# Optimization experiments

Hardware: AMD Instinct MI355X
Metric: run time of the kernel (lower is better)

## Reference

```python
import jax, jax.numpy as jnp
import numpy as np

EPS = 1e-6
SINKHORN_ITERS = 8
TEMPERATURE = 1.0
B, N, D = 4, 8192, 512
E, OUT = 8, 512
H = 1


def setup_inputs() -> dict:
    key = jax.random.key(0)
    k1, k2, k3 = jax.random.split(key, 3)
    x = jax.random.normal(k1, (B, N, D), dtype=jnp.float32)
    gate_weight = jax.random.normal(k2, (H, D, E), dtype=jnp.float32)
    experts = jax.random.normal(k3, (E, D, OUT), dtype=jnp.float32) * 0.02
    return {"x": x, "gate_weight": gate_weight, "experts": experts}


def _sinkhorn(logits):
    # logits: (b, h, n, e). log(clamp(.,eps)) then alternating row/col log-normalization.
    t = jnp.log(jnp.clip(logits, EPS)) / TEMPERATURE
    for _ in range(SINKHORN_ITERS):
        t = t - jax.nn.logsumexp(t, axis=-2, keepdims=True)  # normalize over tokens n
        t = t - jax.nn.logsumexp(t, axis=-1, keepdims=True)  # normalize over experts e
    return jnp.exp(t)


def reference(x, gate_weight, experts):
    b, n, d = x.shape
    e = experts.shape[0]
    m = n // e  # tokens per expert
    xh = x[:, None, :, :]  # b 1 n d  (single-headed -> h=1)
    gate_logits = jnp.einsum('bhnd,hde->bhne', xh, gate_weight)
    gates = _sinkhorn(gate_logits)  # b h n e
    # topk over token dim n, per expert: move n to last axis for lax.top_k
    g_t = jnp.swapaxes(gates, -1, -2)  # b h e n
    vals, idx = jax.lax.top_k(g_t, m)  # (b h e m), (b h e m)
    gate_values = jnp.transpose(vals, (2, 0, 1, 3))[..., None]  # e b h m 1
    # gather routed tokens: routed[e,b,h,m,d] = x[b,h,idx[b,h,e,m],d]
    routed = jnp.take_along_axis(xh[:, :, None, :, :], idx[..., None], axis=3)  # b h e m d
    routed = jnp.transpose(routed, (2, 0, 1, 3, 4))  # e b h m d
    expert_w = experts[:, None, :, :]  # e h i o with h=1 (rearrange 'e i o -> e 1 i o')
    outputs = jnp.einsum('ebhmi,ehio->ebhmo', routed, expert_w)  # e b h m o
    outputs = outputs * gate_values
    # scatter back (set semantics, matching einx set_at)
    bh_idx = idx.reshape(b, 1, e * m)  # b h (e m)
    bh_vals = jnp.transpose(outputs, (1, 2, 0, 3, 4)).reshape(b, 1, e * m, outputs.shape[-1])
    def scat(i1, v1):
        return jnp.zeros((n, v1.shape[-1]), dtype=v1.dtype).at[i1].set(v1)
    routed_back = jax.vmap(jax.vmap(scat))(bh_idx, bh_vals)  # b h n o
    return routed_back[:, 0]  # b n o
```

## Files before the change

kernel.cpp:

```cpp
#include <hip/hip_runtime.h>
#include <hip/hip_bf16.h>

#define BB 4
#define NN 8192
#define DD 512
#define EE 8
#define OUTD 512
#define TOPM 1024
#define EPSV 1e-6f
#define ITERS 8

using s16x8 = __attribute__((ext_vector_type(8))) short;
using f32x4 = __attribute__((ext_vector_type(4))) float;
typedef unsigned long long u64;

__device__ __forceinline__ unsigned short f2bf(float f) {
  unsigned u = __float_as_uint(f);
  return (unsigned short)((u + 0x7FFFu + ((u >> 16) & 1u)) >> 16);
}

__device__ __forceinline__ void gll16(const void* g, void* l) {
  __builtin_amdgcn_global_load_lds((const __attribute__((address_space(1))) void*)g,
                                   (__attribute__((address_space(3))) void*)l, 16, 0, 0);
}

__global__ __launch_bounds__(256) void k_gate(const float* __restrict__ x,
                                              const float* __restrict__ gw,
                                              float* __restrict__ t0,
                                              unsigned short* __restrict__ xbf,
                                              int* __restrict__ eo,
                                              int* __restrict__ counts,
                                              const float* __restrict__ W,
                                              unsigned short* __restrict__ WT) {
  const int tid = threadIdx.x;
  if (blockIdx.x >= 2048) {
    __shared__ float tl[32][33];
    const int widx = blockIdx.x - 2048;
    const int e = widx >> 8, rem = widx & 255;
    const int k0 = (rem >> 4) * 32, n0 = (rem & 15) * 32;
    const int ty = tid >> 5, tx = tid & 31;
    const float* src = W + ((long)e * DD + k0) * OUTD + n0;
#pragma unroll
    for (int j = 0; j < 4; ++j)
      tl[ty + j * 8][tx] = src[(long)(ty + j * 8) * OUTD + tx];
    __syncthreads();
    unsigned short* dst = WT + ((long)e * OUTD + n0) * DD + k0;
#pragma unroll
    for (int j = 0; j < 4; ++j)
      dst[(long)(ty + j * 8) * DD + tx] = f2bf(tl[tx][ty + j * 8]);
    return;
  }
  if (tid < 16) eo[blockIdx.x * 16 + tid] = -1;
  if (blockIdx.x == 0 && tid >= 64 && tid < 64 + BB * EE) counts[tid - 64] = 0;
  const int lane = tid & 63;
  const int w    = tid >> 6;
  float4 g0[8], g1[8];
  const float* gb = gw + (lane * 8) * EE;
#pragma unroll
  for (int q = 0; q < 8; ++q) {
    g0[q] = *(const float4*)(gb + q * EE);
    g1[q] = *(const float4*)(gb + q * EE + 4);
  }
  const long row0 = (long)blockIdx.x * 16 + w * 4;
  float4 xa[4], xb[4];
#pragma unroll
  for (int i = 0; i < 4; ++i) {
    const float* xr = x + (row0 + i) * DD + lane * 8;
    xa[i] = *(const float4*)(xr);
    xb[i] = *(const float4*)(xr + 4);
  }
  float vout[4];
#pragma unroll
  for (int i = 0; i < 4; ++i) {
    float xv[8] = {xa[i].x, xa[i].y, xa[i].z, xa[i].w,
                   xb[i].x, xb[i].y, xb[i].z, xb[i].w};
    s16x8 xo;
#pragma unroll
    for (int j = 0; j < 8; ++j) xo[j] = (short)f2bf(xv[j]);
    *(s16x8*)(xbf + (row0 + i) * DD + lane * 8) = xo;

    float acc[8] = {0.f,0.f,0.f,0.f,0.f,0.f,0.f,0.f};
#pragma unroll
    for (int q = 0; q < 8; ++q) {
      acc[0] += xv[q] * g0[q].x; acc[1] += xv[q] * g0[q].y;
      acc[2] += xv[q] * g0[q].z; acc[3] += xv[q] * g0[q].w;
      acc[4] += xv[q] * g1[q].x; acc[5] += xv[q] * g1[q].y;
      acc[6] += xv[q] * g1[q].z; acc[7] += xv[q] * g1[q].w;
    }
    const bool o1 = lane & 1;
    float own, oth, b0, b1, b2, b3, c0, c1, v;
    own = o1 ? acc[1] : acc[0]; oth = o1 ? acc[0] : acc[1];
    b0 = own + __shfl_xor(oth, 1);
    own = o1 ? acc[3] : acc[2]; oth = o1 ? acc[2] : acc[3];
    b1 = own + __shfl_xor(oth, 1);
    own = o1 ? acc[5] : acc[4]; oth = o1 ? acc[4] : acc[5];
    b2 = own + __shfl_xor(oth, 1);
    own = o1 ? acc[7] : acc[6]; oth = o1 ? acc[6] : acc[7];
    b3 = own + __shfl_xor(oth, 1);
    const bool o2 = lane & 2;
    own = o2 ? b1 : b0; oth = o2 ? b0 : b1;
    c0 = own + __shfl_xor(oth, 2);
    own = o2 ? b3 : b2; oth = o2 ? b2 : b3;
    c1 = own + __shfl_xor(oth, 2);
    const bool o4 = lane & 4;
    own = o4 ? c1 : c0; oth = o4 ? c0 : c1;
    v = own + __shfl_xor(oth, 4);
    v += __shfl_xor(v, 8);
    v += __shfl_xor(v, 16);
    v += __shfl_xor(v, 32);
    vout[i] = v;
  }
  const int gsel = lane >> 3;
  float vsel = vout[0];
  vsel = (gsel == 1) ? vout[1] : vsel;
  vsel = (gsel == 2) ? vout[2] : vsel;
  vsel = (gsel == 3) ? vout[3] : vsel;
  if (lane < 32) t0[row0 * EE + lane] = logf(fmaxf(vsel, EPSV));
}

__global__ __launch_bounds__(1024) void k_sink5(const float* __restrict__ t0,
                                                float* __restrict__ R,
                                                float* __restrict__ C) {
  const int b = blockIdx.x;
  const int tid = threadIdx.x;
  const int wv = tid >> 6, ln = tid & 63;
  const float* tb = t0 + (long)b * NN * EE;
  float E[8][8], u[8], dl[8];
  __shared__ float ws[16][8];
  __shared__ float Csh[8];
  __shared__ float Ssh[8];
#pragma unroll
  for (int j = 0; j < 8; ++j) {
    const float* p = tb + (long)(j * 1024 + tid) * EE;
    float4 a = *(const float4*)p, b4 = *(const float4*)(p + 4);
    E[j][0] = expf(a.x);  E[j][1] = expf(a.y);
    E[j][2] = expf(a.z);  E[j][3] = expf(a.w);
    E[j][4] = expf(b4.x); E[j][5] = expf(b4.y);
    E[j][6] = expf(b4.z); E[j][7] = expf(b4.w);
    u[j] = 1.f;
  }
  for (int it = 0; it < ITERS; ++it) {
    float P[8] = {0.f,0.f,0.f,0.f,0.f,0.f,0.f,0.f};
#pragma unroll
    for (int j = 0; j < 8; ++j)
#pragma unroll
      for (int e = 0; e < 8; ++e) P[e] += E[j][e] * u[j];
#pragma unroll
    for (int d = 1; d <= 4; d <<= 1) {
#pragma unroll
      for (int e = 0; e < 8; ++e) {
        float tmp = __shfl_xor(P[e], d);
        P[e] += ((ln & d) == (e & d)) ? tmp : 0.f;
      }
    }
    float pv = P[0];
#pragma unroll
    for (int e = 1; e < 8; ++e) pv = ((ln & 7) == e) ? P[e] : pv;
#pragma unroll
    for (int d = 8; d < 64; d <<= 1) pv += __shfl_xor(pv, d);
    if (ln < 8) ws[wv][ln] = pv;
    __syncthreads();
    if (tid < 64) {
      const int q = ln >> 3, e = ln & 7;
      float s = ws[q][e] + ws[q + 8][e];
#pragma unroll
      for (int d = 8; d < 64; d <<= 1) s += __shfl_xor(s, d);
      if (ln < 8) { Csh[ln] = 1.f / s; Ssh[ln] = s; }
    }
    __syncthreads();
    float vv[8];
#pragma unroll
    for (int e = 0; e < 8; ++e) vv[e] = Csh[e];
#pragma unroll
    for (int j = 0; j < 8; ++j) {
      float d0 = E[j][0] * vv[0];
#pragma unroll
      for (int e = 1; e < 8; ++e) d0 += E[j][e] * vv[e];
      dl[j] = d0;
      u[j] = 1.f / d0;
    }
    __syncthreads();
  }
#pragma unroll
  for (int j = 0; j < 8; ++j) R[(long)b * NN + j * 1024 + tid] = logf(dl[j]);
  if (tid < 8) C[b * EE + tid] = logf(Ssh[tid]);
}

__global__ __launch_bounds__(1024) void k_topk(const float* __restrict__ t0,
                                               const float* __restrict__ R,
                                               int* __restrict__ expert_of) {
  __shared__ unsigned key[NN];
  __shared__ int hist[256];
  __shared__ int bcast[2];
  __shared__ int wsum[16];
  const int b = blockIdx.x >> 3, e = blockIdx.x & 7;
  const int tid = threadIdx.x;
  const int wv = tid >> 6, ln = tid & 63;
  const float* t = t0 + (long)b * NN * EE + e;
  const float* Rb = R + b * NN;
  for (int n = tid; n < NN; n += 1024) {
    float f = t[n * EE] - Rb[n];
    unsigned u = __float_as_uint(f);
    u = (u & 0x80000000u) ? ~u : (u | 0x80000000u);
    key[n] = u;
  }
  __syncthreads();
  unsigned prefix = 0, mask = 0;
  int k = TOPM;
  for (int shift = 24; shift >= 0; shift -= 8) {
    if (tid < 256) hist[tid] = 0;
    __syncthreads();
    for (int n = tid; n < NN; n += 1024) {
      unsigned u = key[n];
      if ((u & mask) == prefix) atomicAdd(&hist[(u >> shift) & 255], 1);
    }
    __syncthreads();
    for (int d = 1; d < 256; d <<= 1) {
      int add = 0;
      if (tid < 256 - d) add = hist[tid + d];
      __syncthreads();
      if (tid < 256) hist[tid] += add;
      __syncthreads();
    }
    if (tid < 256) {
      int sv = hist[tid];
      int sv1 = (tid < 255) ? hist[tid + 1] : 0;
      if (sv >= k && sv1 < k) { bcast[0] = k - sv1; bcast[1] = tid; }
    }
    __syncthreads();
    k = bcast[0];
    prefix |= ((unsigned)bcast[1]) << shift;
    mask |= (255u << shift);
    __syncthreads();
  }
  const unsigned theta = prefix;
  const int need = k;
  const int base = tid * 8;
  int c = 0;
#pragma unroll
  for (int j = 0; j < 8; ++j) if (key[base + j] == theta) ++c;
  int inc = c;
#pragma unroll
  for (int d = 1; d < 64; d <<= 1) {
    int o = __shfl_up(inc, d);
    if (ln >= d) inc += o;
  }
  if (ln == 63) wsum[wv] = inc;
  __syncthreads();
  if (tid == 0) {
    int runv = 0;
    for (int i = 0; i < 16; ++i) { int t2 = wsum[i]; wsum[i] = runv; runv += t2; }
  }
  __syncthreads();
  int run = wsum[wv] + inc - c;
  int* eo = expert_of + b * NN;
  for (int j = 0; j < 8; ++j) {
    int n = base + j;
    unsigned u = key[n];
    bool sel = false;
    if (u > theta) sel = true;
    else if (u == theta) { if (run < need) sel = true; ++run; }
    if (sel) atomicMax(&eo[n], e);
  }
}

__global__ __launch_bounds__(256) void k_build(const int* __restrict__ expert_of,
                                               const float* __restrict__ t0,
                                               const float* __restrict__ R,
                                               const float* __restrict__ C,
                                               int* __restrict__ counts,
                                               int* __restrict__ lists,
                                               float* __restrict__ gvals) {
  __shared__ int hist8[8], base8[8];
  const int tid = threadIdx.x;
  if (tid < 8) hist8[tid] = 0;
  __syncthreads();
  const long i = (long)blockIdx.x * 256 + tid;
  const int b = (int)(i >> 13);
  const int e = expert_of[i];
  int lpos = -1;
  if (e >= 0) lpos = atomicAdd(&hist8[e], 1);
  __syncthreads();
  if (tid < 8 && hist8[tid] > 0)
    base8[tid] = atomicAdd(&counts[b * EE + tid], hist8[tid]);
  __syncthreads();
  if (e >= 0) {
    const int n = (int)(i & (NN - 1));
    const int be = b * EE + e;
    const int slot = be * TOPM + base8[e] + lpos;
    lists[slot] = n;
    gvals[slot] = expf(t0[i * EE + e] - C[be] - R[i]);
  }
}

__global__ __launch_bounds__(256) void k_zero(const int* __restrict__ eo,
                                              float* __restrict__ out) {
  const int row = blockIdx.x * 4 + (threadIdx.x >> 6);
  if (eo[row] >= 0) return;
  const int ln = threadIdx.x & 63;
  float4 z = make_float4(0.f, 0.f, 0.f, 0.f);
  float4* p = (float4*)(out + (long)row * OUTD) + ln;
  p[0] = z; p[64] = z;
}

__global__ __launch_bounds__(256) void k_gemm(const unsigned short* __restrict__ xbf,
                                              const unsigned short* __restrict__ WT,
                                              const int* __restrict__ counts,
                                              const int* __restrict__ lists,
                                              const float* __restrict__ gvals,
                                              float* __restrict__ out) {
  const int id = blockIdx.x;
  const int xq = id >> 8;
  const int be = (id >> 3) & 31;
  const int yq = id & 7;
  const int b = be >> 3, e = be & 7;
  const int cnt = counts[be];
  const int r0 = yq * 128;
  if (r0 >= cnt) return;
  const int c0 = xq * 128;

  __shared__ unsigned short As[128 * 64];
  __shared__ unsigned short Bs[128 * 64];
  __shared__ int   rowTok[128];
  __shared__ float rowG[128];

  const int tid = threadIdx.x;
  if (tid < 128) {
    int r = r0 + tid;
    rowTok[tid] = (r < cnt) ? lists[be * TOPM + r] : -1;
    rowG[tid]   = (r < cnt) ? gvals[be * TOPM + r] : 0.f;
  }
  __syncthreads();

  const int w = tid >> 6, l = tid & 63;
  const int rbase = w * 32 + (l >> 3);
  const int sL = l & 7;
  const unsigned short* xb_b = xbf + (long)b * NN * DD;
  const unsigned short* wt_e = WT + (long)e * OUTD * DD;
  int tokc[4]; int sGa[4], sGb[4];
#pragma unroll
  for (int c = 0; c < 4; ++c) {
    int r = rbase + c * 8;
    int tk = rowTok[r]; if (tk < 0) tk = 0;
    tokc[c] = tk;
    sGa[c] = (sL ^ (r & 7)) * 8;
    sGb[c] = sGa[c];
  }

  const int wr = w >> 1, wc = w & 1;
  const int fr = l & 15, fq = l >> 4;
  int aoff[4][2], boff[4][2];
#pragma unroll
  for (int m = 0; m < 4; ++m) {
#pragma unroll
    for (int kk = 0; kk < 2; ++kk) {
      int row = wr * 64 + m * 16 + fr;
      aoff[m][kk] = row * 64 + (((fq + 4 * kk) ^ (row & 7)) * 8);
      int col = wc * 64 + m * 16 + fr;
      boff[m][kk] = col * 64 + (((fq + 4 * kk) ^ (col & 7)) * 8);
    }
  }

  f32x4 acc[4][4] = {};

#define STAGE(kb) {                                                          \
    int ko = (kb) * 64;                                                      \
    _Pragma("unroll")                                                        \
    for (int c = 0; c < 4; ++c) {                                            \
      int r = rbase + c * 8;                                                 \
      gll16(xb_b + (long)tokc[c] * DD + ko + sGa[c],                         \
            As + (w * 32 + c * 8) * 64);                                     \
      gll16(wt_e + (long)(c0 + r) * DD + ko + sGb[c],                        \
            Bs + (w * 32 + c * 8) * 64);                                     \
    }                                                                        \
  }

  STAGE(0);
  for (int kb = 0; kb < 8; ++kb) {
    __syncthreads();
    s16x8 af[4][2], bf_[4][2];
#pragma unroll
    for (int m = 0; m < 4; ++m) {
      af[m][0] = *(const s16x8*)(As + aoff[m][0]);
      af[m][1] = *(const s16x8*)(As + aoff[m][1]);
      bf_[m][0] = *(const s16x8*)(Bs + boff[m][0]);
      bf_[m][1] = *(const s16x8*)(Bs + boff[m][1]);
    }
    __syncthreads();
    if (kb < 7) STAGE(kb + 1);
#pragma unroll
    for (int kk = 0; kk < 2; ++kk)
#pragma unroll
      for (int m = 0; m < 4; ++m)
#pragma unroll
        for (int n = 0; n < 4; ++n)
          acc[m][n] = __builtin_amdgcn_mfma_f32_16x16x32_bf16(af[m][kk], bf_[n][kk], acc[m][n], 0, 0, 0);
  }
#undef STAGE

#pragma unroll
  for (int m = 0; m < 4; ++m) {
    int rbase2 = wr * 64 + m * 16 + fq * 4;
    int tok[4]; float g[4];
#pragma unroll
    for (int j = 0; j < 4; ++j) { tok[j] = rowTok[rbase2 + j]; g[j] = rowG[rbase2 + j]; }
#pragma unroll
    for (int n = 0; n < 4; ++n) {
      int col = c0 + wc * 64 + n * 16 + fr;
#pragma unroll
      for (int j = 0; j < 4; ++j) {
        if (tok[j] >= 0)
          out[((long)b * NN + tok[j]) * OUTD + col] = acc[m][n][j] * g[j];
      }
    }
  }
}

extern "C" void kernel_launch(void* const* d_in, const int* in_sizes, int n_in,
                              void* d_out, int out_size, void* d_ws, size_t ws_size,
                              hipStream_t stream) {
  const float* x  = (const float*)d_in[0];
  const float* gw = (const float*)d_in[1];
  const float* ex = (const float*)d_in[2];
  float* out = (float*)d_out;

  char* wsb = (char*)d_ws;
  float*          t0     = (float*)(wsb);
  unsigned short* xbf    = (unsigned short*)(wsb + (1l << 20));
  unsigned short* WT     = (unsigned short*)(wsb + (33l << 20));
  const long base = 37l << 20;
  float*          R      = (float*)(wsb + base);
  int*            eo     = (int*)  (wsb + base + (128l << 10));
  int*            lists  = (int*)  (wsb + base + (256l << 10));
  float*          gvals  = (float*)(wsb + base + (384l << 10));
  float*          C      = (float*)(wsb + base + (512l << 10));
  int*            counts = (int*)  (wsb + base + (512l << 10) + 1024);

  k_gate<<<2048 + 2048, 256, 0, stream>>>(x, gw, t0, xbf, eo, counts, ex, WT);
  k_sink5<<<BB, 1024, 0, stream>>>(t0, R, C);
  k_topk<<<BB * EE, 1024, 0, stream>>>(t0, R, eo);
  k_build<<<(BB * NN) / 256, 256, 0, stream>>>(eo, t0, R, C, counts, lists, gvals);
  k_zero<<<(BB * NN) / 4, 256, 0, stream>>>(eo, out);
  k_gemm<<<1024, 256, 0, stream>>>(xbf, WT, counts, lists, gvals, out);
}
```

Measured before the change: 114.3 us.

## Widen GEMM tile to full output width with double-buffered LDS K-loop

The expert GEMM now has each 512-thread block compute a 128-row by 512-column tile, so each gathered token row is loaded from x once instead of four times. The K loop uses 32-wide slices with double-buffered LDS, issuing the next global-to-LDS load before the current slice's MFMAs and dropping one barrier per iteration. The grid shrinks from 1024 to 256 blocks, which lowers parallelism and raises accumulator register pressure (32 f32x4 per lane).

Result: slower. 117.0 us (+2.3%).

```diff
diff --git a/kernel.cpp b/kernel.cpp
--- a/kernel.cpp
+++ b/kernel.cpp
@@ -303,24 +303,23 @@
   p[0] = z; p[64] = z;
 }
 
-__global__ __launch_bounds__(256) void k_gemm(const unsigned short* __restrict__ xbf,
-                                              const unsigned short* __restrict__ WT,
-                                              const int* __restrict__ counts,
-                                              const int* __restrict__ lists,
-                                              const float* __restrict__ gvals,
-                                              float* __restrict__ out) {
+__global__ __launch_bounds__(512, 2) void k_gemm(const unsigned short* __restrict__ xbf,
+                                                 const unsigned short* __restrict__ WT,
+                                                 const int* __restrict__ counts,
+                                                 const int* __restrict__ lists,
+                                                 const float* __restrict__ gvals,
+                                                 float* __restrict__ out) {
   const int id = blockIdx.x;
-  const int xq = id >> 8;
-  const int be = (id >> 3) & 31;
-  const int yq = id & 7;
-  const int b = be >> 3, e = be & 7;
+  const int e = id & 7;
+  const int b = (id >> 3) & 3;
+  const int yq = id >> 5;
+  const int be = b * EE + e;
   const int cnt = counts[be];
   const int r0 = yq * 128;
   if (r0 >= cnt) return;
-  const int c0 = xq * 128;
-
-  __shared__ unsigned short As[128 * 64];
-  __shared__ unsigned short Bs[128 * 64];
+
+  __shared__ unsigned short As[2][128 * 32];
+  __shared__ unsigned short Bs[2][512 * 32];
   __shared__ int   rowTok[128];
   __shared__ float rowG[128];
 
@@ -333,80 +332,67 @@
   __syncthreads();
 
   const int w = tid >> 6, l = tid & 63;
-  const int rbase = w * 32 + (l >> 3);
-  const int sL = l & 7;
-  const unsigned short* xb_b = xbf + (long)b * NN * DD;
+  const int raS = w * 16 + (l >> 2);
+  int tokA = rowTok[raS]; if (tokA < 0) tokA = 0;
+  const unsigned short* gA = xbf + ((long)b * NN + tokA) * DD + (((l & 3) ^ (raS & 3)) * 8);
   const unsigned short* wt_e = WT + (long)e * OUTD * DD;
-  int tokc[4]; int sGa[4], sGb[4];
+  const unsigned short* gB[4];
 #pragma unroll
   for (int c = 0; c < 4; ++c) {
-    int r = rbase + c * 8;
-    int tk = rowTok[r]; if (tk < 0) tk = 0;
-    tokc[c] = tk;
-    sGa[c] = (sL ^ (r & 7)) * 8;
-    sGb[c] = sGa[c];
-  }
-
-  const int wr = w >> 1, wc = w & 1;
+    int rb = c * 128 + w * 16 + (l >> 2);
+    gB[c] = wt_e + (long)rb * DD + (((l & 3) ^ (rb & 3)) * 8);
+  }
+
   const int fr = l & 15, fq = l >> 4;
-  int aoff[4][2], boff[4][2];
-#pragma unroll
-  for (int m = 0; m < 4; ++m) {
-#pragma unroll
-    for (int kk = 0; kk < 2; ++kk) {
-      int row = wr * 64 + m * 16 + fr;
-      aoff[m][kk] = row * 64 + (((fq + 4 * kk) ^ (row & 7)) * 8);
-      int col = wc * 64 + m * 16 + fr;
-      boff[m][kk] = col * 64 + (((fq + 4 * kk) ^ (col & 7)) * 8);
-    }
-  }
-
-  f32x4 acc[4][4] = {};
-
-#define STAGE(kb) {                                                          \
-    int ko = (kb) * 64;                                                      \
-    _Pragma("unroll")                                                        \
-    for (int c = 0; c < 4; ++c) {                                            \
-      int r = rbase + c * 8;                                                 \
-      gll16(xb_b + (long)tokc[c] * DD + ko + sGa[c],                         \
-            As + (w * 32 + c * 8) * 64);                                     \
-      gll16(wt_e + (long)(c0 + r) * DD + ko + sGb[c],                        \
-            Bs + (w * 32 + c * 8) * 64);                                     \
-    }                                                                        \
-  }
-
-  STAGE(0);
-  for (int kb = 0; kb < 8; ++kb) {
-    __syncthreads();
-    s16x8 af[4][2], bf_[4][2];
-#pragma unroll
-    for (int m = 0; m < 4; ++m) {
-      af[m][0] = *(const s16x8*)(As + aoff[m][0]);
-      af[m][1] = *(const s16x8*)(As + aoff[m][1]);
-      bf_[m][0] = *(const s16x8*)(Bs + boff[m][0]);
-      bf_[m][1] = *(const s16x8*)(Bs + boff[m][1]);
-    }
-    __syncthreads();
-    if (kb < 7) STAGE(kb + 1);
-#pragma unroll
-    for (int kk = 0; kk < 2; ++kk)
-#pragma unroll
-      for (int m = 0; m < 4; ++m)
-#pragma unroll
-        for (int n = 0; n < 4; ++n)
-          acc[m][n] = __builtin_amdgcn_mfma_f32_16x16x32_bf16(af[m][kk], bf_[n][kk], acc[m][n], 0, 0, 0);
+  int aoff[8], boff[4];
+#pragma unroll
+  for (int m = 0; m < 8; ++m) {
+    int row = m * 16 + fr;
+    aoff[m] = row * 32 + ((fq ^ (row & 3)) * 8);
+  }
+#pragma unroll
+  for (int n = 0; n < 4; ++n) {
+    int col = w * 64 + n * 16 + fr;
+    boff[n] = col * 32 + ((fq ^ (col & 3)) * 8);
+  }
+
+  f32x4 acc[8][4] = {};
+
+#define STAGE(kb, p) {                                                        \
+    int ko = (kb) * 32;                                                       \
+    gll16(gA + ko, &As[p][(w * 16) * 32]);                                    \
+    _Pragma("unroll")                                                         \
+    for (int c = 0; c < 4; ++c)                                               \
+      gll16(gB[c] + ko, &Bs[p][(c * 128 + w * 16) * 32]);                     \
+  }
+
+  STAGE(0, 0);
+  for (int kb = 0; kb < 16; ++kb) {
+    const int p = kb & 1;
+    __syncthreads();
+    if (kb < 15) STAGE(kb + 1, p ^ 1);
+    s16x8 af[8], bf_[4];
+#pragma unroll
+    for (int m = 0; m < 8; ++m) af[m] = *(const s16x8*)(&As[p][0] + aoff[m]);
+#pragma unroll
+    for (int n = 0; n < 4; ++n) bf_[n] = *(const s16x8*)(&Bs[p][0] + boff[n]);
+#pragma unroll
+    for (int m = 0; m < 8; ++m)
+#pragma unroll
+      for (int n = 0; n < 4; ++n)
+        acc[m][n] = __builtin_amdgcn_mfma_f32_16x16x32_bf16(af[m], bf_[n], acc[m][n], 0, 0, 0);
   }
 #undef STAGE
 
 #pragma unroll
-  for (int m = 0; m < 4; ++m) {
-    int rbase2 = wr * 64 + m * 16 + fq * 4;
+  for (int m = 0; m < 8; ++m) {
+    int rb2 = m * 16 + fq * 4;
     int tok[4]; float g[4];
 #pragma unroll
-    for (int j = 0; j < 4; ++j) { tok[j] = rowTok[rbase2 + j]; g[j] = rowG[rbase2 + j]; }
+    for (int j = 0; j < 4; ++j) { tok[j] = rowTok[rb2 + j]; g[j] = rowG[rb2 + j]; }
 #pragma unroll
     for (int n = 0; n < 4; ++n) {
-      int col = c0 + wc * 64 + n * 16 + fr;
+      int col = w * 64 + n * 16 + fr;
 #pragma unroll
       for (int j = 0; j < 4; ++j) {
         if (tok[j] >= 0)
@@ -441,5 +427,5 @@
   k_topk<<<BB * EE, 1024, 0, stream>>>(t0, R, eo);
   k_build<<<(BB * NN) / 256, 256, 0, stream>>>(eo, t0, R, C, counts, lists, gvals);
   k_zero<<<(BB * NN) / 4, 256, 0, stream>>>(eo, out);
-  k_gemm<<<1024, 256, 0, stream>>>(xbf, WT, counts, lists, gvals, out);
-}
+  k_gemm<<<256, 512, 0, stream>>>(xbf, WT, counts, lists, gvals, out);
+}
```

## Fuse build and zero kernels, speed up top-k radix select scan, flatten gate weights

Applied to the files above, without the earlier changes.

Merges the list-building and output-zeroing kernels into one launch so the two no longer run back to back. The radix-select histogram scan in k_topk now uses a single-wave shuffle suffix scan instead of a barrier-heavy 256-thread Hillis-Steele scan, and the first-pass histogram is built while the keys are written. Gate weights are loaded into a flat register array pinned with asm barriers. The intent is fewer launches and fewer block-wide syncs, at the cost of higher register pressure in k_gate and a heterogeneous fused kernel.

After: 107.0 us. -6.4%, faster.

```diff
diff --git a/kernel.cpp b/kernel.cpp
--- a/kernel.cpp
+++ b/kernel.cpp
@@ -54,13 +54,17 @@
   if (blockIdx.x == 0 && tid >= 64 && tid < 64 + BB * EE) counts[tid - 64] = 0;
   const int lane = tid & 63;
   const int w    = tid >> 6;
-  float4 g0[8], g1[8];
+  float gwf[64];
   const float* gb = gw + (lane * 8) * EE;
 #pragma unroll
-  for (int q = 0; q < 8; ++q) {
-    g0[q] = *(const float4*)(gb + q * EE);
-    g1[q] = *(const float4*)(gb + q * EE + 4);
-  }
+  for (int q = 0; q < 16; ++q) {
+    float4 t = *(const float4*)(gb + q * 4);
+    gwf[q * 4 + 0] = t.x; gwf[q * 4 + 1] = t.y;
+    gwf[q * 4 + 2] = t.z; gwf[q * 4 + 3] = t.w;
+  }
+#pragma unroll
+  for (int q = 0; q < 64; ++q) asm volatile("" : "+v"(gwf[q]));
+
   const long row0 = (long)blockIdx.x * 16 + w * 4;
   float4 xa[4], xb[4];
 #pragma unroll
@@ -81,12 +85,9 @@
 
     float acc[8] = {0.f,0.f,0.f,0.f,0.f,0.f,0.f,0.f};
 #pragma unroll
-    for (int q = 0; q < 8; ++q) {
-      acc[0] += xv[q] * g0[q].x; acc[1] += xv[q] * g0[q].y;
-      acc[2] += xv[q] * g0[q].z; acc[3] += xv[q] * g0[q].w;
-      acc[4] += xv[q] * g1[q].x; acc[5] += xv[q] * g1[q].y;
-      acc[6] += xv[q] * g1[q].z; acc[7] += xv[q] * g1[q].w;
-    }
+    for (int q = 0; q < 8; ++q)
+#pragma unroll
+      for (int e = 0; e < 8; ++e) acc[e] += xv[q] * gwf[q * 8 + e];
     const bool o1 = lane & 1;
     float own, oth, b0, b1, b2, b3, c0, c1, v;
     own = o1 ? acc[1] : acc[0]; oth = o1 ? acc[0] : acc[1];
@@ -198,39 +199,48 @@
   const int wv = tid >> 6, ln = tid & 63;
   const float* t = t0 + (long)b * NN * EE + e;
   const float* Rb = R + b * NN;
+  if (tid < 256) hist[tid] = 0;
+  __syncthreads();
   for (int n = tid; n < NN; n += 1024) {
     float f = t[n * EE] - Rb[n];
     unsigned u = __float_as_uint(f);
     u = (u & 0x80000000u) ? ~u : (u | 0x80000000u);
     key[n] = u;
+    atomicAdd(&hist[u >> 24], 1);
   }
   __syncthreads();
   unsigned prefix = 0, mask = 0;
   int k = TOPM;
   for (int shift = 24; shift >= 0; shift -= 8) {
-    if (tid < 256) hist[tid] = 0;
-    __syncthreads();
-    for (int n = tid; n < NN; n += 1024) {
-      unsigned u = key[n];
-      if ((u & mask) == prefix) atomicAdd(&hist[(u >> shift) & 255], 1);
-    }
-    __syncthreads();
-    for (int d = 1; d < 256; d <<= 1) {
-      int add = 0;
-      if (tid < 256 - d) add = hist[tid + d];
-      __syncthreads();
-      if (tid < 256) hist[tid] += add;
-      __syncthreads();
-    }
-    if (tid < 256) {
-      int sv = hist[tid];
-      int sv1 = (tid < 255) ? hist[tid + 1] : 0;
-      if (sv >= k && sv1 < k) { bcast[0] = k - sv1; bcast[1] = tid; }
+    if (tid < 64) {
+      const int4 h4 = *(const int4*)&hist[ln * 4];
+      const int r3 = h4.w, r2 = h4.z + r3, r1 = h4.y + r2, r0 = h4.x + r1;
+      int suf = r0;
+#pragma unroll
+      for (int d = 1; d < 64; d <<= 1) {
+        int o = __shfl_down(suf, d);
+        if (ln + d < 64) suf += o;
+      }
+      const int above = suf - r0;
+      const int cum0 = above + r0, cum1 = above + r1;
+      const int cum2 = above + r2, cum3 = above + r3;
+      if (cum0 >= k && cum1 < k) { bcast[0] = k - cum1; bcast[1] = ln * 4 + 0; }
+      if (cum1 >= k && cum2 < k) { bcast[0] = k - cum2; bcast[1] = ln * 4 + 1; }
+      if (cum2 >= k && cum3 < k) { bcast[0] = k - cum3; bcast[1] = ln * 4 + 2; }
+      if (cum3 >= k && above < k) { bcast[0] = k - above; bcast[1] = ln * 4 + 3; }
     }
     __syncthreads();
     k = bcast[0];
     prefix |= ((unsigned)bcast[1]) << shift;
     mask |= (255u << shift);
+    if (shift == 0) break;
+    if (tid < 256) hist[tid] = 0;
+    __syncthreads();
+    const int nsh = shift - 8;
+    for (int n = tid; n < NN; n += 1024) {
+      unsigned u = key[n];
+      if ((u & mask) == prefix) atomicAdd(&hist[(u >> nsh) & 255], 1);
+    }
     __syncthreads();
   }
   const unsigned theta = prefix;
@@ -264,15 +274,25 @@
   }
 }
 
-__global__ __launch_bounds__(256) void k_build(const int* __restrict__ expert_of,
-                                               const float* __restrict__ t0,
-                                               const float* __restrict__ R,
-                                               const float* __restrict__ C,
-                                               int* __restrict__ counts,
-                                               int* __restrict__ lists,
-                                               float* __restrict__ gvals) {
+__global__ __launch_bounds__(256) void k_post(const int* __restrict__ expert_of,
+                                              const float* __restrict__ t0,
+                                              const float* __restrict__ R,
+                                              const float* __restrict__ C,
+                                              int* __restrict__ counts,
+                                              int* __restrict__ lists,
+                                              float* __restrict__ gvals,
+                                              float* __restrict__ out) {
+  const int tid = threadIdx.x;
+  if (blockIdx.x >= 128) {
+    const int row = (blockIdx.x - 128) * 4 + (tid >> 6);
+    if (expert_of[row] >= 0) return;
+    const int ln = tid & 63;
+    float4 z = make_float4(0.f, 0.f, 0.f, 0.f);
+    float4* p = (float4*)(out + (long)row * OUTD) + ln;
+    p[0] = z; p[64] = z;
+    return;
+  }
   __shared__ int hist8[8], base8[8];
-  const int tid = threadIdx.x;
   if (tid < 8) hist8[tid] = 0;
   __syncthreads();
   const long i = (long)blockIdx.x * 256 + tid;
@@ -291,16 +311,6 @@
     lists[slot] = n;
     gvals[slot] = expf(t0[i * EE + e] - C[be] - R[i]);
   }
-}
-
-__global__ __launch_bounds__(256) void k_zero(const int* __restrict__ eo,
-                                              float* __restrict__ out) {
-  const int row = blockIdx.x * 4 + (threadIdx.x >> 6);
-  if (eo[row] >= 0) return;
-  const int ln = threadIdx.x & 63;
-  float4 z = make_float4(0.f, 0.f, 0.f, 0.f);
-  float4* p = (float4*)(out + (long)row * OUTD) + ln;
-  p[0] = z; p[64] = z;
 }
 
 __global__ __launch_bounds__(256) void k_gemm(const unsigned short* __restrict__ xbf,
@@ -439,7 +449,6 @@
   k_gate<<<2048 + 2048, 256, 0, stream>>>(x, gw, t0, xbf, eo, counts, ex, WT);
   k_sink5<<<BB, 1024, 0, stream>>>(t0, R, C);
   k_topk<<<BB * EE, 1024, 0, stream>>>(t0, R, eo);
-  k_build<<<(BB * NN) / 256, 256, 0, stream>>>(eo, t0, R, C, counts, lists, gvals);
-  k_zero<<<(BB * NN) / 4, 256, 0, stream>>>(eo, out);
+  k_post<<<128 + (BB * NN) / 4, 256, 0, stream>>>(eo, t0, R, C, counts, lists, gvals, out);
   k_gemm<<<1024, 256, 0, stream>>>(xbf, WT, counts, lists, gvals, out);
 }
```
